# Performance work log

Hardware: AMD Instinct MI355X
Metric: run time of the kernel (lower is better)

The kernel has to match this reference:

```python
import jax, jax.numpy as jnp
import numpy as np

N = 100_000      # nodes
E = 1_600_000    # edges
EMB = 128        # embedding_size
H = 128          # h_feats
G = 128          # graphs in batch
L = 4            # SAGEConv layers
EPS = 1e-5       # batchnorm eps


def setup_inputs() -> dict:
    key = jax.random.key(0)
    ks = jax.random.split(key, 11)
    in_feat = jax.random.randint(ks[0], (N,), 0, 257)
    src = jax.random.randint(ks[1], (E,), 0, N)
    dst = jax.random.randint(ks[2], (E,), 0, N)
    graph_ids = jnp.sort(jax.random.randint(ks[3], (N,), 0, G))
    s = 1.0 / np.sqrt(H)
    emb = jax.random.normal(ks[4], (257, EMB), jnp.float32) * 0.02
    W_self = jax.random.normal(ks[5], (L, H, H), jnp.float32) * s
    W_neigh = jax.random.normal(ks[6], (L, H, H), jnp.float32) * s
    b = jax.random.normal(ks[7], (L, H), jnp.float32) * 0.01
    gamma = jnp.ones((L, H), jnp.float32)
    beta = jnp.zeros((L, H), jnp.float32)
    prelu_w = jnp.full((L, H), 0.25, jnp.float32)
    return dict(in_feat=in_feat, src=src, dst=dst, graph_ids=graph_ids,
                emb=emb, W_self=W_self, W_neigh=W_neigh, b=b,
                gamma=gamma, beta=beta, prelu_w=prelu_w)


def reference(in_feat, src, dst, graph_ids, emb, W_self, W_neigh, b, gamma, beta, prelu_w):
    n = in_feat.shape[0]
    h = emb[in_feat]  # [N, EMB]
    ones_e = jnp.ones(src.shape[0], h.dtype)
    deg = jnp.clip(jax.ops.segment_sum(ones_e, dst, num_segments=n), 1.0)  # in-degree
    outs = []
    for l in range(L):
        # mean neighbor aggregation (src -> dst)
        agg = jax.ops.segment_sum(h[src], dst, num_segments=n) / deg[:, None]
        rst = h @ W_self[l] + agg @ W_neigh[l] + b[l]
        # PReLU (per-channel), then BatchNorm1d (training-mode batch stats), per DGL SAGEConv order
        rst = jnp.where(rst > 0, rst, prelu_w[l] * rst)
        mu = rst.mean(0)
        var = rst.var(0)
        rst = (rst - mu) * jax.lax.rsqrt(var + EPS) * gamma[l] + beta[l]
        outs.append(rst)
        h = rst
    hcat = jnp.concatenate(outs, axis=1)  # [N, 4H]
    cnt = jnp.clip(jax.ops.segment_sum(jnp.ones(n, hcat.dtype), graph_ids, num_segments=G), 1.0)
    g_vec = jax.ops.segment_sum(hcat, graph_ids, num_segments=G) / cnt[:, None]  # [G, 4H]
    return g_vec
```

## Files before the change

### kernel.cpp

```cpp
#include <hip/hip_runtime.h>
#include <hip/hip_bf16.h>


#define EPS_BN 1e-5f
#define BSH 9
#define BCHUNK 4096
#define PCAP 10240
#define AGG_BLOCKS 2048
#define NPSLOT 64

typedef __attribute__((ext_vector_type(8))) short bf16x8;
typedef __attribute__((ext_vector_type(4))) float f32x4;
typedef __attribute__((address_space(1))) const void gconst_t;
typedef __attribute__((address_space(3))) void ldsv_t;

__global__ __launch_bounds__(256) void k_embed(const int* __restrict__ feat,
                                               const float* __restrict__ emb,
                                               __hip_bfloat162* __restrict__ hb2, int n) {
  int idx = blockIdx.x * 256 + threadIdx.x;
  if (idx < n * 64) {
    int i = idx >> 6, c2 = idx & 63;
    float2 v = ((const float2*)emb)[feat[i] * 64 + c2];
    hb2[idx] = __float22bfloat162_rn(v);
  }
}

__global__ __launch_bounds__(256) void k_wconv(const float* __restrict__ W,
                                               __hip_bfloat16* __restrict__ Wt, int total) {
  int idx = blockIdx.x * 256 + threadIdx.x;
  if (idx < total) {
    int l = idx >> 14, r = idx & 16383, nn = r >> 7, kk = r & 127;
    Wt[idx] = __float2bfloat16(W[(l << 14) + kk * 128 + nn]);
  }
}

__global__ void k_gcount(const int* __restrict__ gid, int* __restrict__ gcnt,
                         int* __restrict__ gstart, int n, int G) {
  int g = blockIdx.x * blockDim.x + threadIdx.x;
  if (g >= G) return;
  int lo0 = 0, hi = n;
  while (lo0 < hi) { int mid = (lo0 + hi) >> 1; if (gid[mid] < g) lo0 = mid + 1; else hi = mid; }
  int lo1 = lo0; hi = n;
  while (lo1 < hi) { int mid = (lo1 + hi) >> 1; if (gid[mid] < g + 1) lo1 = mid + 1; else hi = mid; }
  gstart[g] = lo0;
  gcnt[g] = lo1 - lo0;
}

__global__ __launch_bounds__(256) void k_bhist(const int* __restrict__ dst,
                                               int* __restrict__ bktcnt, int m, int nbkt) {
  __shared__ int h[256];
  int t = threadIdx.x;
  h[t] = 0;
  __syncthreads();
#pragma unroll
  for (int k = 0; k < 4; ++k) {
    int idx = blockIdx.x * BCHUNK + k * 1024 + t * 4;
    if (idx + 4 <= m) {
      int4 d = *(const int4*)&dst[idx];
      atomicAdd(&h[d.x >> BSH], 1);
      atomicAdd(&h[d.y >> BSH], 1);
      atomicAdd(&h[d.z >> BSH], 1);
      atomicAdd(&h[d.w >> BSH], 1);
    } else {
      for (int e = idx; e < m && e < idx + 4; ++e) atomicAdd(&h[dst[e] >> BSH], 1);
    }
  }
  __syncthreads();
  for (int b = t; b < nbkt; b += 256)
    if (h[b]) atomicAdd(&bktcnt[b], h[b]);
}

__global__ void k_bscan(const int* __restrict__ bktcnt, int* __restrict__ bbase,
                        int* __restrict__ bcur, int m, int nbkt) {
  __shared__ int sh[256];
  int t = threadIdx.x;
  int v = (t < nbkt) ? bktcnt[t] : 0;
  sh[t] = v;
  __syncthreads();
  for (int o = 1; o < 256; o <<= 1) {
    int x = (t >= o) ? sh[t - o] : 0;
    __syncthreads();
    sh[t] += x;
    __syncthreads();
  }
  if (t < nbkt) { bbase[t] = sh[t] - v; bcur[t] = sh[t] - v; }
  if (t == 0) bbase[nbkt] = m;
}

__global__ __launch_bounds__(256) void k_bin(const int* __restrict__ src, const int* __restrict__ dst,
                                             int* __restrict__ bcur, uint2* __restrict__ binned,
                                             int m, int nbkt) {
  __shared__ uint2 st[BCHUNK];
  __shared__ int bcnt[256], boff[256], bres[256], wcur[256], ss[256];
  int t = threadIdx.x;
  int e0 = blockIdx.x * BCHUNK;
  int cn = min(BCHUNK, m - e0);
  int sv[16], dv[16];
  for (int b = t; b < 256; b += 256) bcnt[b] = 0;
  __syncthreads();
#pragma unroll
  for (int k = 0; k < 16; ++k) {
    int idx = e0 + k * 256 + t;
    if (idx < e0 + cn) {
      sv[k] = src[idx];
      dv[k] = dst[idx];
      atomicAdd(&bcnt[dv[k] >> BSH], 1);
    } else dv[k] = -1;
  }
  __syncthreads();
  int v = (t < nbkt) ? bcnt[t] : 0;
  ss[t] = v;
  __syncthreads();
  for (int o = 1; o < 256; o <<= 1) {
    int x = (t >= o) ? ss[t - o] : 0;
    __syncthreads();
    ss[t] += x;
    __syncthreads();
  }
  if (t < nbkt) {
    int ex = ss[t] - v;
    boff[t] = ex;
    wcur[t] = ex;
    if (v) bres[t] = atomicAdd(&bcur[t], v);
  }
  __syncthreads();
#pragma unroll
  for (int k = 0; k < 16; ++k) {
    if (dv[k] >= 0) {
      int b = dv[k] >> BSH;
      int p = atomicAdd(&wcur[b], 1);
      st[p] = make_uint2((unsigned)sv[k], (unsigned)dv[k]);
    }
  }
  __syncthreads();
  for (int j = t; j < cn; j += 256) {
    uint2 e = st[j];
    int b = (int)(e.y >> BSH);
    binned[(size_t)bres[b] + (j - boff[b])] = e;
  }
}

__global__ __launch_bounds__(256) void k_cnt(const uint2* __restrict__ binned,
                                             const int* __restrict__ bbase,
                                             int* __restrict__ cnt, int n) {
  __shared__ int h[512];
  int b = blockIdx.x, t = threadIdx.x;
  int base = b << BSH;
  int nn = min(512, n - base);
  h[t] = 0; h[t + 256] = 0;
  __syncthreads();
  int lo = bbase[b], hi = bbase[b + 1];
  for (int j = lo + t; j < hi; j += 256) atomicAdd(&h[(int)binned[j].y - base], 1);
  __syncthreads();
  if (t < nn) cnt[base + t] = h[t];
  if (t + 256 < nn) cnt[base + t + 256] = h[t + 256];
}

__global__ __launch_bounds__(256) void k_scan1(const int* __restrict__ cnt,
                                               int* __restrict__ excl,
                                               int* __restrict__ blk_sums, int n) {
  __shared__ int sh[256];
  int t = threadIdx.x;
  int base = blockIdx.x * 1024 + t * 4;
  int4 v = {0, 0, 0, 0};
  if (base < n) v = *(const int4*)&cnt[base];
  int s = v.x + v.y + v.z + v.w;
  sh[t] = s;
  __syncthreads();
  for (int off = 1; off < 256; off <<= 1) {
    int x = (t >= off) ? sh[t - off] : 0;
    __syncthreads();
    sh[t] += x;
    __syncthreads();
  }
  int ex = sh[t] - s;
  if (t == 255) blk_sums[blockIdx.x] = sh[255];
  if (base < n) {
    excl[base]     = ex;
    excl[base + 1] = ex + v.x;
    excl[base + 2] = ex + v.x + v.y;
    excl[base + 3] = ex + v.x + v.y + v.z;
  }
}

__global__ void k_scan2(int* __restrict__ bs, int nb) {
  __shared__ int sh[128];
  int t = threadIdx.x;
  int v = (t < nb) ? bs[t] : 0;
  sh[t] = v;
  __syncthreads();
  for (int off = 1; off < 128; off <<= 1) {
    int x = (t >= off) ? sh[t - off] : 0;
    __syncthreads();
    sh[t] += x;
    __syncthreads();
  }
  if (t < nb) bs[t] = sh[t] - v;
}

__global__ __launch_bounds__(256) void k_scan3(int* __restrict__ rp, const int* __restrict__ bs,
                                               const int* __restrict__ cnt, int* __restrict__ cursor,
                                               float* __restrict__ deg, int n, int ne) {
  int i = blockIdx.x * 256 + threadIdx.x;
  if (i < n) {
    int r = rp[i] + bs[i >> 10];
    rp[i] = r;
    cursor[i] = r;
    int c = cnt[i];
    deg[i] = (float)(c > 0 ? c : 1);
  }
  if (i == 0) rp[n] = ne;
}

__global__ __launch_bounds__(256) void k_place(const uint2* __restrict__ binned,
                                               const int* __restrict__ bbase,
                                               const int* __restrict__ rp,
                                               int* __restrict__ cursor,
                                               int* __restrict__ csr_src, int n) {
  int b = blockIdx.x, t = threadIdx.x;
  int base = b << BSH;
  int lo = bbase[b], hi = bbase[b + 1], m = hi - lo;
  if (m <= 0) return;
  if (m > PCAP) {
    for (int j = lo + t; j < hi; j += 256) {
      uint2 e = binned[j];
      int p = atomicAdd(&cursor[(int)e.y], 1);
      csr_src[p] = (int)e.x;
    }
    return;
  }
  __shared__ int h[512], loff[512], wc[512], ss[256];
  __shared__ int stage[PCAP];
  h[t] = 0; h[t + 256] = 0;
  __syncthreads();
  for (int j = lo + t; j < hi; j += 256) atomicAdd(&h[(int)binned[j].y - base], 1);
  __syncthreads();
  int a0 = h[2 * t], a1 = h[2 * t + 1];
  int s = a0 + a1;
  ss[t] = s;
  __syncthreads();
  for (int o = 1; o < 256; o <<= 1) {
    int x = (t >= o) ? ss[t - o] : 0;
    __syncthreads();
    ss[t] += x;
    __syncthreads();
  }
  int ex = ss[t] - s;
  loff[2 * t] = ex; loff[2 * t + 1] = ex + a0;
  wc[2 * t] = ex;   wc[2 * t + 1] = ex + a0;
  __syncthreads();
  for (int j = lo + t; j < hi; j += 256) {
    uint2 e = binned[j];
    int p = atomicAdd(&wc[(int)e.y - base], 1);
    stage[p] = (int)e.x;
  }
  __syncthreads();
  int cb = rp[base];
  for (int j = t; j < m; j += 256) csr_src[cb + j] = stage[j];
}

__global__ __launch_bounds__(256) void k_prep(const float* __restrict__ b0,
                                              float* __restrict__ ss0,
                                              float* __restrict__ beffS0,
                                              float* __restrict__ cN0,
                                              const uint4* __restrict__ Wst0,
                                              const uint4* __restrict__ Wnt0,
                                              uint4* __restrict__ Ws2,
                                              uint4* __restrict__ Wn2) {
  int id = blockIdx.x * 256 + threadIdx.x;
  if (id < 128) {
    ss0[id] = 1.f; ss0[128 + id] = 0.f;
    beffS0[id] = b0[id]; cN0[id] = 0.f;
  }
  int half = id >> 11, ch = id & 2047;
  if (half) Wn2[ch] = Wnt0[ch]; else Ws2[ch] = Wst0[ch];
}

__global__ __launch_bounds__(256) void k_gemm2(
    const __hip_bfloat16* __restrict__ hb,
    const __hip_bfloat16* __restrict__ Wst2, const __hip_bfloat16* __restrict__ Wnt2,
    __hip_bfloat16* __restrict__ Ys, __hip_bfloat16* __restrict__ Yn, int n) {
  __shared__ short Ah[128 * 128];
  int t = threadIdx.x;
  int row0 = blockIdx.x * 128;
  int w = t >> 6, lane = t & 63;

#pragma unroll
  for (int rd = 0; rd < 8; ++rd) {
    int Gq = rd * 256 + w * 64 + lane;
    int r = Gq >> 4;
    int gq = (Gq & 15) ^ (r & 7);
    int grow = row0 + r;
    grow = grow < n ? grow : n - 1;
    const __hip_bfloat16* gs = hb + (size_t)grow * 128 + gq * 8;
    __builtin_amdgcn_global_load_lds((gconst_t*)gs,
        (ldsv_t*)&Ah[(rd * 256 + w * 64) * 8], 16, 0, 0);
  }
  asm volatile("s_waitcnt vmcnt(0)" ::: "memory");
  __syncthreads();

  int lr16 = lane & 15, hi = lane >> 4;
  const __hip_bfloat16* Bt[2] = {Wst2, Wnt2};
  __hip_bfloat16* Ot[2] = {Ys, Yn};
#pragma unroll
  for (int s = 0; s < 2; ++s) {
    const __hip_bfloat16* B = Bt[s];
    f32x4 acc[2][8];
#pragma unroll
    for (int fm = 0; fm < 2; ++fm)
#pragma unroll
      for (int fn = 0; fn < 8; ++fn) acc[fm][fn] = (f32x4){0.f, 0.f, 0.f, 0.f};
#pragma unroll
    for (int ks = 0; ks < 4; ++ks) {
      bf16x8 af[2], bfr[8];
#pragma unroll
      for (int fm = 0; fm < 2; ++fm) {
        int rl = w * 32 + fm * 16 + lr16;
        int gq = (ks * 4 + hi) ^ (lr16 & 7);
        af[fm] = *(const bf16x8*)&Ah[rl * 128 + gq * 8];
      }
#pragma unroll
      for (int fn = 0; fn < 8; ++fn)
        bfr[fn] = *(const bf16x8*)(B + (size_t)(fn * 16 + lr16) * 128 + ks * 32 + hi * 8);
#pragma unroll
      for (int fm = 0; fm < 2; ++fm)
#pragma unroll
        for (int fn = 0; fn < 8; ++fn)
          acc[fm][fn] = __builtin_amdgcn_mfma_f32_16x16x32_bf16(af[fm], bfr[fn], acc[fm][fn], 0, 0, 0);
    }
    __hip_bfloat16* O = Ot[s];
#pragma unroll
    for (int fm = 0; fm < 2; ++fm) {
      int rbase = row0 + w * 32 + fm * 16 + hi * 4;
#pragma unroll
      for (int fn = 0; fn < 8; ++fn) {
        int col = fn * 16 + lr16;
#pragma unroll
        for (int r = 0; r < 4; ++r) {
          int grow = rbase + r;
          if (grow < n) O[(size_t)grow * 128 + col] = __float2bfloat16(acc[fm][fn][r]);
        }
      }
    }
  }
}

__device__ __forceinline__ void acc8(float* a, uint4 v) {
  float2 f;
  f = __bfloat1622float2(*(const __hip_bfloat162*)&v.x); a[0] += f.x; a[1] += f.y;
  f = __bfloat1622float2(*(const __hip_bfloat162*)&v.y); a[2] += f.x; a[3] += f.y;
  f = __bfloat1622float2(*(const __hip_bfloat162*)&v.z); a[4] += f.x; a[5] += f.y;
  f = __bfloat1622float2(*(const __hip_bfloat162*)&v.w); a[6] += f.x; a[7] += f.y;
}

__global__ __launch_bounds__(256) void k_aggfin(
    const uint4* __restrict__ yn4, const int* __restrict__ rp,
    const int* __restrict__ csr_src, const float* __restrict__ deg,
    const uint4* __restrict__ ys4,
    const float* __restrict__ beffS, const float* __restrict__ cN,
    const float* __restrict__ pw,
    uint4* __restrict__ hbn4, float* __restrict__ partial, int n) {
  __shared__ float ls[128], lq[128];
  int t = threadIdx.x;
  int lane = t & 63, wid = t >> 6;
  int g = lane >> 4, lr = lane & 15;
  if (t < 128) { ls[t] = 0.f; lq[t] = 0.f; }
  __syncthreads();

  float bS[8], cn8[8], pw8[8], sacc[8], qacc[8];
#pragma unroll
  for (int c = 0; c < 8; ++c) {
    bS[c] = beffS[lr * 8 + c];
    cn8[c] = cN[lr * 8 + c];
    pw8[c] = pw[lr * 8 + c];
    sacc[c] = 0.f; qacc[c] = 0.f;
  }

  for (int i = blockIdx.x * 4 + wid; i < n; i += gridDim.x * 4) {
    int beg = rp[i], end = rp[i + 1];
    float a[8];
#pragma unroll
    for (int c = 0; c < 8; ++c) a[c] = 0.f;
    int e = beg;
    for (; e + 8 <= end; e += 8) {
      int s0 = csr_src[e + g];
      int s1 = csr_src[e + 4 + g];
      uint4 v0 = yn4[(size_t)s0 * 16 + lr];
      uint4 v1 = yn4[(size_t)s1 * 16 + lr];
      acc8(a, v0);
      acc8(a, v1);
    }
    for (; e + g < end; e += 4) {
      int s = csr_src[e + g];
      uint4 v = yn4[(size_t)s * 16 + lr];
      acc8(a, v);
    }
#pragma unroll
    for (int c = 0; c < 8; ++c) {
      a[c] += __shfl_xor(a[c], 16, 64);
      a[c] += __shfl_xor(a[c], 32, 64);
    }
    if (g == 0) {
      uint4 ysv = ys4[(size_t)i * 16 + lr];
      float y[8];
      float2 f;
      f = __bfloat1622float2(*(const __hip_bfloat162*)&ysv.x); y[0] = f.x; y[1] = f.y;
      f = __bfloat1622float2(*(const __hip_bfloat162*)&ysv.y); y[2] = f.x; y[3] = f.y;
      f = __bfloat1622float2(*(const __hip_bfloat162*)&ysv.z); y[4] = f.x; y[5] = f.y;
      f = __bfloat1622float2(*(const __hip_bfloat162*)&ysv.w); y[6] = f.x; y[7] = f.y;
      float invd = 1.0f / deg[i];
      bool has = (beg < end);
      float v[8];
#pragma unroll
      for (int c = 0; c < 8; ++c) {
        float x = y[c] + bS[c];
        if (has) x += a[c] * invd + cn8[c];
        x = x > 0.f ? x : pw8[c] * x;
        sacc[c] += x; qacc[c] += x * x;
        v[c] = x;
      }
      __hip_bfloat162 p0 = __float22bfloat162_rn(make_float2(v[0], v[1]));
      __hip_bfloat162 p1 = __float22bfloat162_rn(make_float2(v[2], v[3]));
      __hip_bfloat162 p2 = __float22bfloat162_rn(make_float2(v[4], v[5]));
      __hip_bfloat162 p3 = __float22bfloat162_rn(make_float2(v[6], v[7]));
      uint4 o;
      o.x = *(unsigned int*)&p0; o.y = *(unsigned int*)&p1;
      o.z = *(unsigned int*)&p2; o.w = *(unsigned int*)&p3;
      hbn4[(size_t)i * 16 + lr] = o;
    }
  }
  if (g == 0) {
#pragma unroll
    for (int c = 0; c < 8; ++c) {
      atomicAdd(&ls[lr * 8 + c], sacc[c]);
      atomicAdd(&lq[lr * 8 + c], qacc[c]);
    }
  }
  __syncthreads();
  if (t < 128) {
    float* pp = partial + (size_t)(blockIdx.x >> 5) * 256;
    atomicAdd(&pp[t], ls[t]);
    atomicAdd(&pp[128 + t], lq[t]);
  }
}

__global__ __launch_bounds__(1024) void k_bnfin(float* __restrict__ partial, int nb,
                                                const float* __restrict__ gamma,
                                                const float* __restrict__ beta,
                                                float* __restrict__ ss,
                                                const float* __restrict__ bias_next,
                                                const float* __restrict__ Wsf_next,
                                                const float* __restrict__ Wnf_next,
                                                const __hip_bfloat16* __restrict__ Wst_next,
                                                const __hip_bfloat16* __restrict__ Wnt_next,
                                                __hip_bfloat16* __restrict__ Ws2,
                                                __hip_bfloat16* __restrict__ Wn2,
                                                float* __restrict__ beffS_next,
                                                float* __restrict__ cN_next,
                                                int has_next, int n) {
  __shared__ float red[4][256];
  __shared__ float shv[128], scv[128];
  __shared__ float bredS[8][128], bredN[8][128];
  int t = threadIdx.x, c = t & 255, part = t >> 8;
  float s = 0.f;
  for (int b = part; b < nb; b += 4) s += partial[(size_t)b * 256 + c];
  red[part][c] = s;
  __syncthreads();
  if (part == 0) red[0][c] = red[0][c] + red[1][c] + red[2][c] + red[3][c];
  __syncthreads();
  if (t < 128) {
    float inv_n = 1.0f / (float)n;
    float mu = red[0][t] * inv_n;
    float var = red[0][128 + t] * inv_n - mu * mu;
    float sc = rsqrtf(var + EPS_BN) * gamma[t];
    float sh = beta[t] - mu * sc;
    ss[t] = sc;
    ss[128 + t] = sh;
    shv[t] = sh;
    scv[t] = sc;
  }
  __syncthreads();
  if (has_next) {
    int cc = t & 127, kg = t >> 7;
    float aS = 0.f, aN = 0.f;
#pragma unroll
    for (int k = kg * 16; k < kg * 16 + 16; ++k) {
      float sh = shv[k];
      aS += sh * Wsf_next[k * 128 + cc];
      aN += sh * Wnf_next[k * 128 + cc];
    }
    bredS[kg][cc] = aS;
    bredN[kg][cc] = aN;
    __syncthreads();
    if (t < 128) {
      float rS = bias_next[t], rN = 0.f;
#pragma unroll
      for (int kg2 = 0; kg2 < 8; ++kg2) { rS += bredS[kg2][t]; rN += bredN[kg2][t]; }
      beffS_next[t] = rS;
      cN_next[t] = rN;
    }
    for (int i = t; i < 16384; i += 1024) {
      float scf = scv[i & 127];
      Ws2[i] = __float2bfloat16(__bfloat162float(Wst_next[i]) * scf);
      Wn2[i] = __float2bfloat16(__bfloat162float(Wnt_next[i]) * scf);
    }
  }
  for (int i = t; i < nb * 256; i += 1024) partial[i] = 0.f;
}

__global__ __launch_bounds__(256) void k_pool(const uint4* __restrict__ hb4,
                                              const int* __restrict__ gstart,
                                              const int* __restrict__ gcnt,
                                              float* __restrict__ out, int l) {
  __shared__ float red[4][128];
  int g = blockIdx.x >> 3, c = blockIdx.x & 7;
  int len = gcnt[g];
  int i0 = gstart[g] + ((len * c) >> 3);
  int i1 = gstart[g] + ((len * (c + 1)) >> 3);
  if (i0 >= i1) return;
  int t = threadIdx.x, w = t >> 6, lane = t & 63;
  int gi = lane >> 4, lr = lane & 15;
  float a[8];
#pragma unroll
  for (int cc = 0; cc < 8; ++cc) a[cc] = 0.f;
#pragma unroll 2
  for (int r = i0 + w * 4 + gi; r < i1; r += 16) {
    uint4 v = hb4[(size_t)r * 16 + lr];
    acc8(a, v);
  }
#pragma unroll
  for (int cc = 0; cc < 8; ++cc) {
    a[cc] += __shfl_xor(a[cc], 16, 64);
    a[cc] += __shfl_xor(a[cc], 32, 64);
  }
  if (gi == 0) {
#pragma unroll
    for (int cc = 0; cc < 8; ++cc) red[w][lr * 8 + cc] = a[cc];
  }
  __syncthreads();
  if (t < 128)
    atomicAdd(&out[(size_t)g * 512 + l * 128 + t],
              red[0][t] + red[1][t] + red[2][t] + red[3][t]);
}

__global__ __launch_bounds__(256) void k_div(float* __restrict__ out, const int* __restrict__ gcnt,
                                             const float* __restrict__ ssbuf, int m) {
  int i = blockIdx.x * 256 + threadIdx.x;
  if (i < m) {
    int g = i >> 9;
    int lc = i & 511;
    int l = lc >> 7, c = lc & 127;
    const float* ss = ssbuf + (l + 1) * 256;
    int cn = gcnt[g];
    out[i] = (cn > 0) ? (out[i] / (float)cn) * ss[c] + ss[128 + c] : 0.f;
  }
}

extern "C" void kernel_launch(void* const* d_in, const int* in_sizes, int n_in,
                              void* d_out, int out_size, void* d_ws, size_t ws_size,
                              hipStream_t stream) {
  const int*   in_feat = (const int*)d_in[0];
  const int*   src     = (const int*)d_in[1];
  const int*   dst     = (const int*)d_in[2];
  const int*   gid     = (const int*)d_in[3];
  const float* emb     = (const float*)d_in[4];
  const float* Wself   = (const float*)d_in[5];
  const float* Wneigh  = (const float*)d_in[6];
  const float* bvec    = (const float*)d_in[7];
  const float* gamma   = (const float*)d_in[8];
  const float* beta    = (const float*)d_in[9];
  const float* prelu   = (const float*)d_in[10];
  const int N = in_sizes[0];
  const int E = in_sizes[1];
  const int G = out_size / 512;
  float* out = (float*)d_out;
  const int NB = (N + 127) / 128;
  const int NBKT = (N + 511) >> BSH;

  char* p = (char*)d_ws;
  size_t off = 0;
  auto take = [&](size_t bytes) { void* r = p + off; off += (bytes + 255) & ~(size_t)255; return r; };
  __hip_bfloat16* hb0   = (__hip_bfloat16*)take((size_t)N * 128 * 2);
  __hip_bfloat16* hb1   = (__hip_bfloat16*)take((size_t)N * 128 * 2);
  __hip_bfloat16* Ysb   = (__hip_bfloat16*)take((size_t)N * 128 * 2);
  __hip_bfloat16* Ynb   = (__hip_bfloat16*)take((size_t)N * 128 * 2);
  __hip_bfloat16* Wst   = (__hip_bfloat16*)take((size_t)4 * 128 * 128 * 2);
  __hip_bfloat16* Wnt   = (__hip_bfloat16*)take((size_t)4 * 128 * 128 * 2);
  __hip_bfloat16* Wst2  = (__hip_bfloat16*)take((size_t)128 * 128 * 2);
  __hip_bfloat16* Wnt2  = (__hip_bfloat16*)take((size_t)128 * 128 * 2);
  float* partial        = (float*)take((size_t)NPSLOT * 256 * 4);
  float* ssbuf          = (float*)take((size_t)5 * 256 * 4);
  float* beffS          = (float*)take((size_t)4 * 128 * 4);
  float* cNb            = (float*)take((size_t)4 * 128 * 4);
  uint2* binned  = (uint2*)take((size_t)E * 8);
  int*   csr_src = (int*)take((size_t)E * 4);
  int*   cnt     = (int*)take((size_t)N * 4);
  int*   rp      = (int*)take((size_t)(N + 1) * 4);
  int*   cursor  = (int*)take((size_t)N * 4);
  float* deg     = (float*)take((size_t)N * 4);
  int*   bs      = (int*)take(512);
  int*   gcnt    = (int*)take((size_t)G * 4);
  int*   gstart  = (int*)take((size_t)G * 4);
  int*   bktcnt  = (int*)take((size_t)NBKT * 4);
  int*   bbase   = (int*)take((size_t)(NBKT + 1) * 4);
  int*   bcur    = (int*)take((size_t)NBKT * 4);
  if (off > ws_size) return;

  hipMemsetAsync(bktcnt, 0, (size_t)NBKT * 4, stream);
  hipMemsetAsync(partial, 0, (size_t)NPSLOT * 256 * 4, stream);
  hipMemsetAsync(d_out, 0, (size_t)out_size * 4, stream);

  k_embed<<<(N * 64 + 255) / 256, 256, 0, stream>>>(in_feat, emb, (__hip_bfloat162*)hb0, N);
  k_wconv<<<(4 * 128 * 128 + 255) / 256, 256, 0, stream>>>(Wself, Wst, 4 * 128 * 128);
  k_wconv<<<(4 * 128 * 128 + 255) / 256, 256, 0, stream>>>(Wneigh, Wnt, 4 * 128 * 128);
  k_gcount<<<1, 128, 0, stream>>>(gid, gcnt, gstart, N, G);

  int nbb = (E + BCHUNK - 1) / BCHUNK;
  k_bhist<<<nbb, 256, 0, stream>>>(dst, bktcnt, E, NBKT);
  k_bscan<<<1, 256, 0, stream>>>(bktcnt, bbase, bcur, E, NBKT);
  k_bin<<<nbb, 256, 0, stream>>>(src, dst, bcur, binned, E, NBKT);
  k_cnt<<<NBKT, 256, 0, stream>>>(binned, bbase, cnt, N);
  int nsb = (N + 1023) / 1024;
  k_scan1<<<nsb, 256, 0, stream>>>(cnt, rp, bs, N);
  k_scan2<<<1, 128, 0, stream>>>(bs, nsb);
  k_scan3<<<(N + 255) / 256, 256, 0, stream>>>(rp, bs, cnt, cursor, deg, N, E);
  k_place<<<NBKT, 256, 0, stream>>>(binned, bbase, rp, cursor, csr_src, N);
  k_prep<<<16, 256, 0, stream>>>(bvec, ssbuf, beffS, cNb,
                                 (const uint4*)Wst, (const uint4*)Wnt,
                                 (uint4*)Wst2, (uint4*)Wnt2);

  __hip_bfloat16* bufs[2] = {hb0, hb1};
  for (int l = 0; l < 4; ++l) {
    __hip_bfloat16* hin  = bufs[l & 1];
    __hip_bfloat16* hout = bufs[(l + 1) & 1];
    k_gemm2<<<NB, 256, 0, stream>>>(hin, Wst2, Wnt2, Ysb, Ynb, N);
    k_aggfin<<<AGG_BLOCKS, 256, 0, stream>>>((const uint4*)Ynb, rp, csr_src, deg,
                                             (const uint4*)Ysb,
                                             beffS + l * 128, cNb + l * 128,
                                             prelu + l * 128,
                                             (uint4*)hout, partial, N);
    k_bnfin<<<1, 1024, 0, stream>>>(partial, NPSLOT, gamma + l * 128, beta + l * 128,
                                    ssbuf + (l + 1) * 256,
                                    bvec + ((l + 1) & 3) * 128,
                                    Wself + ((l + 1) & 3) * 16384,
                                    Wneigh + ((l + 1) & 3) * 16384,
                                    Wst + ((l + 1) & 3) * 16384,
                                    Wnt + ((l + 1) & 3) * 16384,
                                    Wst2, Wnt2,
                                    beffS + ((l + 1) & 3) * 128,
                                    cNb + ((l + 1) & 3) * 128,
                                    (l < 3) ? 1 : 0, N);
    k_pool<<<G * 8, 256, 0, stream>>>((const uint4*)hout, gstart, gcnt, out, l);
  }
  k_div<<<(out_size + 255) / 256, 256, 0, stream>>>(out, gcnt, ssbuf, out_size);
}
```

Baseline: 698.1 us.

## Split aggregation from epilogue and fuse PReLU/BN-stats with graph pooling

The fused aggregate+activation kernel is split. A pure neighbor-mean kernel now writes the normalized aggregate to the no-longer-needed input buffer. A new per-graph kernel then applies bias, PReLU and the BN statistics, and also does the graph-sum pooling, which replaces the separate pool pass that re-read the layer output. This removes one full read of the activation per layer and the shared-memory atomics. In exchange it adds a write and read of the aggregate buffer, and rounds the aggregate to bf16 before the epilogue.

```diff
diff --git a/kernel.cpp b/kernel.cpp
--- a/kernel.cpp
+++ b/kernel.cpp
@@ -7,7 +7,6 @@
 #define BCHUNK 4096
 #define PCAP 10240
 #define AGG_BLOCKS 2048
-#define NPSLOT 64
 
 typedef __attribute__((ext_vector_type(8))) short bf16x8;
 typedef __attribute__((ext_vector_type(4))) float f32x4;
@@ -353,29 +352,13 @@
   f = __bfloat1622float2(*(const __hip_bfloat162*)&v.w); a[6] += f.x; a[7] += f.y;
 }
 
-__global__ __launch_bounds__(256) void k_aggfin(
-    const uint4* __restrict__ yn4, const int* __restrict__ rp,
-    const int* __restrict__ csr_src, const float* __restrict__ deg,
-    const uint4* __restrict__ ys4,
-    const float* __restrict__ beffS, const float* __restrict__ cN,
-    const float* __restrict__ pw,
-    uint4* __restrict__ hbn4, float* __restrict__ partial, int n) {
-  __shared__ float ls[128], lq[128];
-  int t = threadIdx.x;
-  int lane = t & 63, wid = t >> 6;
+__global__ __launch_bounds__(256) void k_agg(const uint4* __restrict__ yn4,
+                                             const int* __restrict__ rp,
+                                             const int* __restrict__ csr_src,
+                                             const float* __restrict__ deg,
+                                             uint4* __restrict__ aggY4, int n) {
+  int lane = threadIdx.x & 63, wid = threadIdx.x >> 6;
   int g = lane >> 4, lr = lane & 15;
-  if (t < 128) { ls[t] = 0.f; lq[t] = 0.f; }
-  __syncthreads();
-
-  float bS[8], cn8[8], pw8[8], sacc[8], qacc[8];
-#pragma unroll
-  for (int c = 0; c < 8; ++c) {
-    bS[c] = beffS[lr * 8 + c];
-    cn8[c] = cN[lr * 8 + c];
-    pw8[c] = pw[lr * 8 + c];
-    sacc[c] = 0.f; qacc[c] = 0.f;
-  }
-
   for (int i = blockIdx.x * 4 + wid; i < n; i += gridDim.x * 4) {
     int beg = rp[i], end = rp[i + 1];
     float a[8];
@@ -401,46 +384,97 @@
       a[c] += __shfl_xor(a[c], 32, 64);
     }
     if (g == 0) {
-      uint4 ysv = ys4[(size_t)i * 16 + lr];
-      float y[8];
-      float2 f;
-      f = __bfloat1622float2(*(const __hip_bfloat162*)&ysv.x); y[0] = f.x; y[1] = f.y;
-      f = __bfloat1622float2(*(const __hip_bfloat162*)&ysv.y); y[2] = f.x; y[3] = f.y;
-      f = __bfloat1622float2(*(const __hip_bfloat162*)&ysv.z); y[4] = f.x; y[5] = f.y;
-      f = __bfloat1622float2(*(const __hip_bfloat162*)&ysv.w); y[6] = f.x; y[7] = f.y;
       float invd = 1.0f / deg[i];
-      bool has = (beg < end);
-      float v[8];
-#pragma unroll
-      for (int c = 0; c < 8; ++c) {
-        float x = y[c] + bS[c];
-        if (has) x += a[c] * invd + cn8[c];
-        x = x > 0.f ? x : pw8[c] * x;
-        sacc[c] += x; qacc[c] += x * x;
-        v[c] = x;
-      }
-      __hip_bfloat162 p0 = __float22bfloat162_rn(make_float2(v[0], v[1]));
-      __hip_bfloat162 p1 = __float22bfloat162_rn(make_float2(v[2], v[3]));
-      __hip_bfloat162 p2 = __float22bfloat162_rn(make_float2(v[4], v[5]));
-      __hip_bfloat162 p3 = __float22bfloat162_rn(make_float2(v[6], v[7]));
+      __hip_bfloat162 p0 = __float22bfloat162_rn(make_float2(a[0] * invd, a[1] * invd));
+      __hip_bfloat162 p1 = __float22bfloat162_rn(make_float2(a[2] * invd, a[3] * invd));
+      __hip_bfloat162 p2 = __float22bfloat162_rn(make_float2(a[4] * invd, a[5] * invd));
+      __hip_bfloat162 p3 = __float22bfloat162_rn(make_float2(a[6] * invd, a[7] * invd));
       uint4 o;
       o.x = *(unsigned int*)&p0; o.y = *(unsigned int*)&p1;
       o.z = *(unsigned int*)&p2; o.w = *(unsigned int*)&p3;
-      hbn4[(size_t)i * 16 + lr] = o;
-    }
-  }
-  if (g == 0) {
-#pragma unroll
-    for (int c = 0; c < 8; ++c) {
-      atomicAdd(&ls[lr * 8 + c], sacc[c]);
-      atomicAdd(&lq[lr * 8 + c], qacc[c]);
+      aggY4[(size_t)i * 16 + lr] = o;
+    }
+  }
+}
+
+__global__ __launch_bounds__(256) void k_finpool(
+    const uint4* __restrict__ ys4, const uint4* __restrict__ aggY4,
+    const int* __restrict__ cnt,
+    const float* __restrict__ beffS, const float* __restrict__ cN,
+    const float* __restrict__ pw,
+    const int* __restrict__ gstart, const int* __restrict__ gcnt,
+    uint4* __restrict__ hbn4, float* __restrict__ out,
+    float* __restrict__ partial, int l, int n) {
+  __shared__ float redS[4][128], redQ[4][128];
+  int g = blockIdx.x >> 3, c = blockIdx.x & 7;
+  int len = gcnt[g];
+  int i0 = gstart[g] + ((len * c) >> 3);
+  int i1 = gstart[g] + ((len * (c + 1)) >> 3);
+  if (i0 >= i1) return;
+  int t = threadIdx.x, w = t >> 6, lane = t & 63;
+  int gi = lane >> 4, lr = lane & 15;
+  float bS[8], cn8[8], pw8[8], S[8], Q[8];
+#pragma unroll
+  for (int k = 0; k < 8; ++k) {
+    bS[k] = beffS[lr * 8 + k];
+    cn8[k] = cN[lr * 8 + k];
+    pw8[k] = pw[lr * 8 + k];
+    S[k] = 0.f; Q[k] = 0.f;
+  }
+  for (int r = i0 + w * 4 + gi; r < i1; r += 16) {
+    uint4 ys = ys4[(size_t)r * 16 + lr];
+    uint4 ag = aggY4[(size_t)r * 16 + lr];
+    bool has = cnt[r] > 0;
+    float y[8], a[8];
+    float2 f;
+    f = __bfloat1622float2(*(const __hip_bfloat162*)&ys.x); y[0] = f.x; y[1] = f.y;
+    f = __bfloat1622float2(*(const __hip_bfloat162*)&ys.y); y[2] = f.x; y[3] = f.y;
+    f = __bfloat1622float2(*(const __hip_bfloat162*)&ys.z); y[4] = f.x; y[5] = f.y;
+    f = __bfloat1622float2(*(const __hip_bfloat162*)&ys.w); y[6] = f.x; y[7] = f.y;
+    f = __bfloat1622float2(*(const __hip_bfloat162*)&ag.x); a[0] = f.x; a[1] = f.y;
+    f = __bfloat1622float2(*(const __hip_bfloat162*)&ag.y); a[2] = f.x; a[3] = f.y;
+    f = __bfloat1622float2(*(const __hip_bfloat162*)&ag.z); a[4] = f.x; a[5] = f.y;
+    f = __bfloat1622float2(*(const __hip_bfloat162*)&ag.w); a[6] = f.x; a[7] = f.y;
+    float x[8];
+#pragma unroll
+    for (int k = 0; k < 8; ++k) {
+      float xx = y[k] + bS[k];
+      if (has) xx += a[k] + cn8[k];
+      xx = xx > 0.f ? xx : pw8[k] * xx;
+      S[k] += xx; Q[k] += xx * xx;
+      x[k] = xx;
+    }
+    __hip_bfloat162 p0 = __float22bfloat162_rn(make_float2(x[0], x[1]));
+    __hip_bfloat162 p1 = __float22bfloat162_rn(make_float2(x[2], x[3]));
+    __hip_bfloat162 p2 = __float22bfloat162_rn(make_float2(x[4], x[5]));
+    __hip_bfloat162 p3 = __float22bfloat162_rn(make_float2(x[6], x[7]));
+    uint4 o;
+    o.x = *(unsigned int*)&p0; o.y = *(unsigned int*)&p1;
+    o.z = *(unsigned int*)&p2; o.w = *(unsigned int*)&p3;
+    hbn4[(size_t)r * 16 + lr] = o;
+  }
+#pragma unroll
+  for (int k = 0; k < 8; ++k) {
+    S[k] += __shfl_xor(S[k], 16, 64);
+    S[k] += __shfl_xor(S[k], 32, 64);
+    Q[k] += __shfl_xor(Q[k], 16, 64);
+    Q[k] += __shfl_xor(Q[k], 32, 64);
+  }
+  if (gi == 0) {
+#pragma unroll
+    for (int k = 0; k < 8; ++k) {
+      redS[w][lr * 8 + k] = S[k];
+      redQ[w][lr * 8 + k] = Q[k];
     }
   }
   __syncthreads();
   if (t < 128) {
+    float s = redS[0][t] + redS[1][t] + redS[2][t] + redS[3][t];
+    float q = redQ[0][t] + redQ[1][t] + redQ[2][t] + redQ[3][t];
+    atomicAdd(&out[(size_t)g * 512 + l * 128 + t], s);
     float* pp = partial + (size_t)(blockIdx.x >> 5) * 256;
-    atomicAdd(&pp[t], ls[t]);
-    atomicAdd(&pp[128 + t], lq[t]);
+    atomicAdd(&pp[t], s);
+    atomicAdd(&pp[128 + t], q);
   }
 }
 
@@ -508,41 +542,6 @@
   for (int i = t; i < nb * 256; i += 1024) partial[i] = 0.f;
 }
 
-__global__ __launch_bounds__(256) void k_pool(const uint4* __restrict__ hb4,
-                                              const int* __restrict__ gstart,
-                                              const int* __restrict__ gcnt,
-                                              float* __restrict__ out, int l) {
-  __shared__ float red[4][128];
-  int g = blockIdx.x >> 3, c = blockIdx.x & 7;
-  int len = gcnt[g];
-  int i0 = gstart[g] + ((len * c) >> 3);
-  int i1 = gstart[g] + ((len * (c + 1)) >> 3);
-  if (i0 >= i1) return;
-  int t = threadIdx.x, w = t >> 6, lane = t & 63;
-  int gi = lane >> 4, lr = lane & 15;
-  float a[8];
-#pragma unroll
-  for (int cc = 0; cc < 8; ++cc) a[cc] = 0.f;
-#pragma unroll 2
-  for (int r = i0 + w * 4 + gi; r < i1; r += 16) {
-    uint4 v = hb4[(size_t)r * 16 + lr];
-    acc8(a, v);
-  }
-#pragma unroll
-  for (int cc = 0; cc < 8; ++cc) {
-    a[cc] += __shfl_xor(a[cc], 16, 64);
-    a[cc] += __shfl_xor(a[cc], 32, 64);
-  }
-  if (gi == 0) {
-#pragma unroll
-    for (int cc = 0; cc < 8; ++cc) red[w][lr * 8 + cc] = a[cc];
-  }
-  __syncthreads();
-  if (t < 128)
-    atomicAdd(&out[(size_t)g * 512 + l * 128 + t],
-              red[0][t] + red[1][t] + red[2][t] + red[3][t]);
-}
-
 __global__ __launch_bounds__(256) void k_div(float* __restrict__ out, const int* __restrict__ gcnt,
                                              const float* __restrict__ ssbuf, int m) {
   int i = blockIdx.x * 256 + threadIdx.x;
@@ -575,6 +574,7 @@
   const int G = out_size / 512;
   float* out = (float*)d_out;
   const int NB = (N + 127) / 128;
+  const int NP = (G * 8 + 31) / 32;
   const int NBKT = (N + 511) >> BSH;
 
   char* p = (char*)d_ws;
@@ -588,7 +588,7 @@
   __hip_bfloat16* Wnt   = (__hip_bfloat16*)take((size_t)4 * 128 * 128 * 2);
   __hip_bfloat16* Wst2  = (__hip_bfloat16*)take((size_t)128 * 128 * 2);
   __hip_bfloat16* Wnt2  = (__hip_bfloat16*)take((size_t)128 * 128 * 2);
-  float* partial        = (float*)take((size_t)NPSLOT * 256 * 4);
+  float* partial        = (float*)take((size_t)NP * 256 * 4);
   float* ssbuf          = (float*)take((size_t)5 * 256 * 4);
   float* beffS          = (float*)take((size_t)4 * 128 * 4);
   float* cNb            = (float*)take((size_t)4 * 128 * 4);
@@ -607,7 +607,7 @@
   if (off > ws_size) return;
 
   hipMemsetAsync(bktcnt, 0, (size_t)NBKT * 4, stream);
-  hipMemsetAsync(partial, 0, (size_t)NPSLOT * 256 * 4, stream);
+  hipMemsetAsync(partial, 0, (size_t)NP * 256 * 4, stream);
   hipMemsetAsync(d_out, 0, (size_t)out_size * 4, stream);
 
   k_embed<<<(N * 64 + 255) / 256, 256, 0, stream>>>(in_feat, emb, (__hip_bfloat162*)hb0, N);
@@ -634,12 +634,13 @@
     __hip_bfloat16* hin  = bufs[l & 1];
     __hip_bfloat16* hout = bufs[(l + 1) & 1];
     k_gemm2<<<NB, 256, 0, stream>>>(hin, Wst2, Wnt2, Ysb, Ynb, N);
-    k_aggfin<<<AGG_BLOCKS, 256, 0, stream>>>((const uint4*)Ynb, rp, csr_src, deg,
-                                             (const uint4*)Ysb,
-                                             beffS + l * 128, cNb + l * 128,
-                                             prelu + l * 128,
-                                             (uint4*)hout, partial, N);
-    k_bnfin<<<1, 1024, 0, stream>>>(partial, NPSLOT, gamma + l * 128, beta + l * 128,
+    k_agg<<<AGG_BLOCKS, 256, 0, stream>>>((const uint4*)Ynb, rp, csr_src, deg,
+                                          (uint4*)hin, N);
+    k_finpool<<<G * 8, 256, 0, stream>>>((const uint4*)Ysb, (const uint4*)hin, cnt,
+                                         beffS + l * 128, cNb + l * 128,
+                                         prelu + l * 128, gstart, gcnt,
+                                         (uint4*)hout, out, partial, l, N);
+    k_bnfin<<<1, 1024, 0, stream>>>(partial, NP, gamma + l * 128, beta + l * 128,
                                     ssbuf + (l + 1) * 256,
                                     bvec + ((l + 1) & 3) * 128,
                                     Wself + ((l + 1) & 3) * 16384,
@@ -650,7 +651,6 @@
                                     beffS + ((l + 1) & 3) * 128,
                                     cNb + ((l + 1) & 3) * 128,
                                     (l < 3) ? 1 : 0, N);
-    k_pool<<<G * 8, 256, 0, stream>>>((const uint4*)hout, gstart, gcnt, out, l);
   }
   k_div<<<(out_size + 255) / 256, 256, 0, stream>>>(out, gcnt, ssbuf, out_size);
 }
```

Result: faster. 596.6 us (-14.5%).
